# Performance work log

Hardware: AMD Instinct MI355X
Metric: run time of the kernel (lower is better)

The kernel has to match this reference:

```python
import jax, jax.numpy as jnp
import numpy as np

D_MODEL = 1024
D_STATE = 128
EXPAND = 2
HEADDIM = 64
D_CONV = 4
VAR_NUM = 3
D_INNER = EXPAND * D_MODEL            # 2048
NHEADS = D_INNER // HEADDIM           # 32
CONV_DIM = D_INNER + 2 * D_STATE      # 2304 (x, B, C share the conv)
D_IN_PROJ = 2 * D_INNER + 2 * D_STATE + NHEADS  # 4384


def setup_inputs() -> dict:
    key = jax.random.key(0)
    ks = jax.random.split(key, 10)
    s = 0.02
    B, L = 4, 2048
    return {
        "h_prev": jax.random.normal(ks[0], (B, L, D_MODEL), jnp.float32),
        "emb_next": jax.random.normal(ks[1], (B, L, D_MODEL), jnp.float32),
        "norm_w": jnp.ones((D_MODEL,), jnp.float32),
        "proj_W": jax.random.normal(ks[2], (D_MODEL, 2 * D_MODEL), jnp.float32) * s,
        "proj_b": jnp.zeros((D_MODEL,), jnp.float32),
        "in_proj_W": jax.random.normal(ks[3], (D_IN_PROJ, D_MODEL), jnp.float32) * s,
        "conv_w": jax.random.normal(ks[4], (CONV_DIM, D_CONV), jnp.float32) * s,
        "conv_b": jnp.zeros((CONV_DIM,), jnp.float32),
        "dt_bias": jax.random.uniform(ks[5], (NHEADS,), jnp.float32) * 0.1,
        "A_log": jnp.log(jnp.arange(1, NHEADS + 1, dtype=jnp.float32)),
        "D": jnp.ones((NHEADS,), jnp.float32),
        "gnorm_w": jnp.ones((D_INNER,), jnp.float32),
        "out_proj_W": jax.random.normal(ks[6], (D_MODEL, D_INNER), jnp.float32) * s,
        "dec_W": jax.random.normal(ks[7], (VAR_NUM, D_MODEL), jnp.float32) * s,
        "dec_b": jnp.zeros((VAR_NUM,), jnp.float32),
    }


def rmsnorm(x, w, eps=1e-6):
    xf = x.astype(jnp.float32)
    v = jnp.mean(jnp.square(xf), axis=-1, keepdims=True)
    return w * (xf * jax.lax.rsqrt(v + eps)).astype(x.dtype)


def gated_rmsnorm(y, z, w, eps=1e-5):
    y = y * jax.nn.silu(z)
    v = jnp.mean(jnp.square(y.astype(jnp.float32)), axis=-1, keepdims=True)
    return w * (y.astype(jnp.float32) * jax.lax.rsqrt(v + eps)).astype(y.dtype)


def mamba2(u, in_proj_W, conv_w, conv_b, dt_bias, A_log, D, gnorm_w, out_proj_W):
    B, L, _ = u.shape
    zxbcdt = u @ in_proj_W.T  # [B,L,D_IN_PROJ]
    z, xBC, dt = jnp.split(zxbcdt, [D_INNER, D_INNER + CONV_DIM], axis=-1)
    # causal depthwise conv over time
    lhs = jnp.moveaxis(xBC, -1, 1)               # [B,C,L]
    rhs = conv_w[:, None, :]                     # [C,1,K]
    conv = jax.lax.conv_general_dilated(lhs, rhs, (1,), [(D_CONV - 1, 0)],
                                        feature_group_count=CONV_DIM)
    xBC = jax.nn.silu(jnp.moveaxis(conv, 1, -1) + conv_b)
    x, Bm, Cm = jnp.split(xBC, [D_INNER, D_INNER + D_STATE], axis=-1)
    x = x.reshape(B, L, NHEADS, HEADDIM)         # [B,L,H,P]
    dt = jax.nn.softplus(dt + dt_bias)           # [B,L,H]
    A = -jnp.exp(A_log)                          # [H]
    dA = jnp.exp(dt * A)                         # [B,L,H]

    def step(state, inp):
        dA_t, dt_t, B_t, C_t, x_t = inp          # [B,H],[B,H],[B,N],[B,N],[B,H,P]
        state = state * dA_t[..., None, None] + (dt_t[..., None, None] * x_t[..., None]) * B_t[:, None, None, :]
        y_t = jnp.einsum('bhpn,bn->bhp', state, C_t)
        return state, y_t

    init = jnp.zeros((B, NHEADS, HEADDIM, D_STATE), u.dtype)
    xs = (jnp.moveaxis(dA, 1, 0), jnp.moveaxis(dt, 1, 0), jnp.moveaxis(Bm, 1, 0),
          jnp.moveaxis(Cm, 1, 0), jnp.moveaxis(x, 1, 0))
    _, y = jax.lax.scan(step, init, xs)          # y: [L,B,H,P]
    y = jnp.moveaxis(y, 0, 1) + D[None, None, :, None] * x
    y = y.reshape(B, L, D_INNER)
    y = gated_rmsnorm(y, z, gnorm_w)
    return y @ out_proj_W.T                      # [B,L,D_MODEL]


def reference(h_prev, emb_next, norm_w, proj_W, proj_b, in_proj_W, conv_w, conv_b,
              dt_bias, A_log, D, gnorm_w, out_proj_W, dec_W, dec_b):
    combined = jnp.concatenate([rmsnorm(h_prev, norm_w), rmsnorm(emb_next, norm_w)], axis=-1)
    h_prime = combined @ proj_W.T + proj_b       # [B,L,D_MODEL]
    h_k = mamba2(h_prime, in_proj_W, conv_w, conv_b, dt_bias, A_log, D, gnorm_w, out_proj_W)
    output = h_k @ dec_W.T + dec_b               # [B,L,VAR_NUM]
    return output, h_k
```

## Files before the change

### kernel.cpp

```cpp
#include <hip/hip_runtime.h>
#include <stdint.h>

#define T_TOK 8192
#define SEQL  2048
#define DM    1024
#define DI    2048
#define DSTATE 128
#define NH    32
#define HD    64
#define CONVD 2304
#define DINP  4384
#define LD_ZX 4480
#define QC    64
#define NCH   32

typedef __attribute__((ext_vector_type(8))) __bf16 bfrag;
typedef __attribute__((ext_vector_type(8))) short s16x8;
typedef __attribute__((ext_vector_type(4))) float f32x4;

__device__ __forceinline__ float bf2f(unsigned short u){
  return __uint_as_float(((unsigned)u) << 16);
}
__device__ __forceinline__ unsigned short f2bf(float f){
  unsigned u = __float_as_uint(f);
  unsigned r = (u + 0x7FFFu + ((u >> 16) & 1u)) >> 16;
  return (unsigned short)r;
}

__device__ __forceinline__ void gl_lds16(const unsigned short* g, unsigned short* l){
  __builtin_amdgcn_global_load_lds(
      (const __attribute__((address_space(1))) void*)g,
      (__attribute__((address_space(3))) void*)l,
      16, 0, 0);
}
__device__ __forceinline__ void gl_lds4(const float* g, float* l){
  __builtin_amdgcn_global_load_lds(
      (const __attribute__((address_space(1))) void*)g,
      (__attribute__((address_space(3))) void*)l,
      4, 0, 0);
}

__global__ __launch_bounds__(256) void cvt_w_kernel(const float* __restrict__ src,
                                                    unsigned short* __restrict__ dst,
                                                    int n4, int srcn4){
  int i = blockIdx.x * 256 + threadIdx.x;
  if (i >= n4) return;
  ushort4 o;
  if (i < srcn4){
    float4 v = ((const float4*)src)[i];
    o.x = f2bf(v.x); o.y = f2bf(v.y); o.z = f2bf(v.z); o.w = f2bf(v.w);
  } else {
    o.x = o.y = o.z = o.w = 0;
  }
  *(ushort4*)(dst + (size_t)i * 4) = o;
}

__global__ __launch_bounds__(256) void rmsnorm2_kernel(const float* __restrict__ a,
                                                       const float* __restrict__ b,
                                                       const float* __restrict__ w,
                                                       unsigned short* __restrict__ out){
  int t = blockIdx.x, tid = threadIdx.x;
  float4 va = *(const float4*)(a + (size_t)t * DM + tid * 4);
  float4 vb = *(const float4*)(b + (size_t)t * DM + tid * 4);
  float sa = va.x*va.x + va.y*va.y + va.z*va.z + va.w*va.w;
  float sb = vb.x*vb.x + vb.y*vb.y + vb.z*vb.z + vb.w*vb.w;
  #pragma unroll
  for (int o = 32; o; o >>= 1){ sa += __shfl_down(sa, o); sb += __shfl_down(sb, o); }
  __shared__ float reda[4], redb[4];
  int wv = tid >> 6, lane = tid & 63;
  if (!lane){ reda[wv] = sa; redb[wv] = sb; }
  __syncthreads();
  float ta = reda[0] + reda[1] + reda[2] + reda[3];
  float tb = redb[0] + redb[1] + redb[2] + redb[3];
  float ra = rsqrtf(ta * (1.f/1024.f) + 1e-6f);
  float rb = rsqrtf(tb * (1.f/1024.f) + 1e-6f);
  float4 vw = *(const float4*)(w + tid * 4);
  unsigned short* o0 = out + (size_t)t * DI + tid * 4;
  o0[0] = f2bf(va.x*ra*vw.x); o0[1] = f2bf(va.y*ra*vw.y);
  o0[2] = f2bf(va.z*ra*vw.z); o0[3] = f2bf(va.w*ra*vw.w);
  unsigned short* o1 = o0 + DM;
  o1[0] = f2bf(vb.x*rb*vw.x); o1[1] = f2bf(vb.y*rb*vw.y);
  o1[2] = f2bf(vb.z*rb*vw.z); o1[3] = f2bf(vb.w*rb*vw.w);
}

template<bool F32OUT>
__global__ __launch_bounds__(256) void gemm_bf16_kernel(const unsigned short* __restrict__ A,
                                                        const unsigned short* __restrict__ W,
                                                        void* __restrict__ Cv,
                                                        const float* __restrict__ bias,
                                                        int M, int N, int K, int ldc){
  __shared__ unsigned short As[128 * 64];
  __shared__ unsigned short Bs[128 * 64];
  const int nN = N >> 7;
  int bid = blockIdx.x;
  const int cpx = gridDim.x >> 3;
  bid = (bid & 7) * cpx + (bid >> 3);
  const int tm = bid / nN, tn = bid % nN;
  const int tid = threadIdx.x;
  const int wv = tid >> 6, lane = tid & 63;
  const int wm = wv >> 1, wn = wv & 1;
  const int rA = lane >> 3;
  const int cA = (lane & 7) << 3;
  const size_t arow0 = (size_t)(tm * 128) * K;
  const size_t brow0 = (size_t)(tn * 128) * K;

  f32x4 zero4 = {0.f, 0.f, 0.f, 0.f};
  f32x4 acc[4][4];
  #pragma unroll
  for (int i = 0; i < 4; ++i)
    #pragma unroll
    for (int j = 0; j < 4; ++j) acc[i][j] = zero4;

  const int nK = K >> 6;
  for (int kt = 0; kt < nK; ++kt){
    const int k0 = kt << 6;
    if (kt) __syncthreads();
    #pragma unroll
    for (int i = 0; i < 4; ++i){
      int base = (wv * 4 + i) * 8;
      gl_lds16(A + arow0 + (size_t)(base + rA) * K + k0 + cA, &As[base * 64]);
      gl_lds16(W + brow0 + (size_t)(base + rA) * K + k0 + cA, &Bs[base * 64]);
    }
    __syncthreads();
    #pragma unroll
    for (int kk = 0; kk < 2; ++kk){
      const int ko = kk * 32 + (lane >> 4) * 8;
      bfrag af[4], bfv[4];
      #pragma unroll
      for (int f = 0; f < 4; ++f){
        af[f]  = *reinterpret_cast<const bfrag*>(&As[(wm*64 + f*16 + (lane & 15)) * 64 + ko]);
        bfv[f] = *reinterpret_cast<const bfrag*>(&Bs[(wn*64 + f*16 + (lane & 15)) * 64 + ko]);
      }
      #pragma unroll
      for (int fm = 0; fm < 4; ++fm)
        #pragma unroll
        for (int fn = 0; fn < 4; ++fn)
          acc[fm][fn] = __builtin_amdgcn_mfma_f32_16x16x32_bf16(af[fm], bfv[fn], acc[fm][fn], 0, 0, 0);
    }
  }
  const int r0 = (lane >> 4) * 4, ci = lane & 15;
  #pragma unroll
  for (int fm = 0; fm < 4; ++fm){
    #pragma unroll
    for (int fn = 0; fn < 4; ++fn){
      int col = tn*128 + wn*64 + fn*16 + ci;
      float bv = bias ? bias[col] : 0.f;
      #pragma unroll
      for (int r = 0; r < 4; ++r){
        int row = tm*128 + wm*64 + fm*16 + r0 + r;
        float val = acc[fm][fn][r] + bv;
        if (F32OUT) ((float*)Cv)[(size_t)row * ldc + col] = val;
        else        ((unsigned short*)Cv)[(size_t)row * ldc + col] = f2bf(val);
      }
    }
  }
}

__global__ __launch_bounds__(256) void conv_kernel(const unsigned short* __restrict__ zx,
                                                   const float* __restrict__ cw,
                                                   const float* __restrict__ cb,
                                                   unsigned short* __restrict__ xbc){
  int c = blockIdx.x * 256 + threadIdx.x;
  int tg = blockIdx.y * 8;
  int l0 = tg & (SEQL - 1);
  const unsigned short* base = zx + (size_t)tg * LD_ZX + DI + c;
  float v[11];
  #pragma unroll
  for (int i = 0; i < 11; ++i){
    int ll = l0 - 3 + i;
    v[i] = (ll >= 0) ? bf2f(base[(ptrdiff_t)(i - 3) * LD_ZX]) : 0.f;
  }
  float w0 = cw[c*4+0], w1 = cw[c*4+1], w2 = cw[c*4+2], w3 = cw[c*4+3];
  float cbv = cb[c];
  unsigned short* ob = xbc + (size_t)tg * CONVD + c;
  #pragma unroll
  for (int s = 0; s < 8; ++s){
    float acc = cbv + w0*v[s] + w1*v[s+1] + w2*v[s+2] + w3*v[s+3];
    float sv = acc / (1.f + expf(-acc));
    ob[(size_t)s * CONVD] = f2bf(sv);
  }
}

__global__ __launch_bounds__(256) void cum_kernel(const unsigned short* __restrict__ zx,
                                                  const float* __restrict__ dtbias,
                                                  const float* __restrict__ alog,
                                                  float* __restrict__ cumT,
                                                  float* __restrict__ dtT,
                                                  float* __restrict__ decayG){
  int gw = blockIdx.x * 4 + (threadIdx.x >> 6);
  int l = threadIdx.x & 63;
  int c = gw & 31, h = (gw >> 5) & 31, b = gw >> 10;
  size_t t = (size_t)b * SEQL + c * QC + l;
  float xr = bf2f(zx[t * LD_ZX + 4352 + h]) + dtbias[h];
  float dt = (xr > 20.f) ? xr : log1pf(expf(xr));
  float A = -expf(alog[h]);
  float x = dt * A;
  #pragma unroll
  for (int d = 1; d < 64; d <<= 1){
    float y = __shfl_up(x, d);
    if (l >= d) x += y;
  }
  size_t o = ((size_t)(b * NH + h)) * SEQL + c * QC + l;
  cumT[o] = x;
  dtT[o] = dt;
  float tot = __shfl(x, 63);
  if (l == 0) decayG[(b * NH + h) * NCH + c] = expf(tot);
}

__global__ __launch_bounds__(256) void chunk_dS_kernel(const unsigned short* __restrict__ xbc,
                                                       const float* __restrict__ cumT,
                                                       const float* __restrict__ dtT,
                                                       unsigned short* __restrict__ dS){
  __shared__ unsigned short Xw[64 * 64];
  __shared__ unsigned short Bt[128 * 64];
  __shared__ float cumS[64], dtS[64];
  const int blk = blockIdx.x;
  const int c = blk & 31, h = (blk >> 5) & 31, b = blk >> 10;
  const int tid = threadIdx.x;
  const int wv = tid >> 6, l = tid & 63;
  const size_t tokB = (size_t)b * SEQL + c * QC;
  const int bh = b * NH + h;

  if (wv == 0) gl_lds4(cumT + (size_t)bh * SEQL + c * QC + l, cumS);
  if (wv == 1) gl_lds4(dtT  + (size_t)bh * SEQL + c * QC + l, dtS);

  const int j = tid >> 2, g4 = tid & 3;
  const unsigned short* xsrc = xbc + (tokB + j) * CONVD + h * HD + g4 * 16;
  s16x8 x0 = *(const s16x8*)xsrc, x1 = *(const s16x8*)(xsrc + 8);
  const unsigned short* bsrc = xbc + (tokB + j) * CONVD + DI + g4 * 32;
  s16x8 b0 = *(const s16x8*)bsrc,        b1 = *(const s16x8*)(bsrc + 8);
  s16x8 b2 = *(const s16x8*)(bsrc + 16), b3 = *(const s16x8*)(bsrc + 24);
  __syncthreads();

  float wj = expf(cumS[63] - cumS[j]) * dtS[j];
  const int jh = (j >> 3), jl = (j & 7);
  #pragma unroll
  for (int e = 0; e < 8; ++e){
    int p = g4 * 16 + e;
    Xw[p * 64 + ((jh ^ (p & 7)) << 3) + jl] = f2bf(bf2f((unsigned short)x0[e]) * wj);
    int p2 = p + 8;
    Xw[p2 * 64 + ((jh ^ (p2 & 7)) << 3) + jl] = f2bf(bf2f((unsigned short)x1[e]) * wj);
  }
  #pragma unroll
  for (int e = 0; e < 8; ++e){
    int n0 = g4 * 32 + e;
    Bt[(n0     ) * 64 + ((jh ^ ((n0     ) & 7)) << 3) + jl] = (unsigned short)b0[e];
    Bt[(n0 +  8) * 64 + ((jh ^ ((n0 +  8) & 7)) << 3) + jl] = (unsigned short)b1[e];
    Bt[(n0 + 16) * 64 + ((jh ^ ((n0 + 16) & 7)) << 3) + jl] = (unsigned short)b2[e];
    Bt[(n0 + 24) * 64 + ((jh ^ ((n0 + 24) & 7)) << 3) + jl] = (unsigned short)b3[e];
  }
  __syncthreads();

  f32x4 z4 = {0.f,0.f,0.f,0.f};
  f32x4 acc[4][2];
  #pragma unroll
  for (int pt = 0; pt < 4; ++pt){ acc[pt][0] = z4; acc[pt][1] = z4; }
  #pragma unroll
  for (int ks = 0; ks < 2; ++ks){
    const int au = ((ks * 4 + (l >> 4)) ^ (l & 7));
    bfrag a[4], bb[2];
    #pragma unroll
    for (int pt = 0; pt < 4; ++pt)
      a[pt] = *(const bfrag*)&Xw[(pt * 16 + (l & 15)) * 64 + au * 8];
    #pragma unroll
    for (int nt = 0; nt < 2; ++nt)
      bb[nt] = *(const bfrag*)&Bt[((wv * 2 + nt) * 16 + (l & 15)) * 64 + au * 8];
    #pragma unroll
    for (int pt = 0; pt < 4; ++pt)
      #pragma unroll
      for (int nt = 0; nt < 2; ++nt)
        acc[pt][nt] = __builtin_amdgcn_mfma_f32_16x16x32_bf16(a[pt], bb[nt], acc[pt][nt], 0, 0, 0);
  }
  unsigned short* out = dS + ((size_t)(bh * NCH + c) * 64) * 128;
  #pragma unroll
  for (int pt = 0; pt < 4; ++pt)
    #pragma unroll
    for (int nt = 0; nt < 2; ++nt)
      #pragma unroll
      for (int r = 0; r < 4; ++r){
        int p = pt * 16 + (l >> 4) * 4 + r;
        int n = (wv * 2 + nt) * 16 + (l & 15);
        out[(size_t)p * 128 + n] = f2bf(acc[pt][nt][r]);
      }
}

__global__ __launch_bounds__(256) void chunk_state_kernel(const float* __restrict__ decayG,
                                                          unsigned short* __restrict__ dS){
  int i = blockIdx.x * 256 + threadIdx.x;
  int n = i & 127, p = (i >> 7) & 63, bh = i >> 13;
  float s = 0.f;
  #pragma unroll 4
  for (int c = 0; c < NCH; ++c){
    size_t idx = ((size_t)(bh * NCH + c) * 64 + p) * 128 + n;
    unsigned short d = dS[idx];
    dS[idx] = f2bf(s);
    s = decayG[bh * NCH + c] * s + bf2f(d);
  }
}

__global__ __launch_bounds__(256) void chunk_Y_kernel(const unsigned short* __restrict__ xbc,
                                                      const unsigned short* __restrict__ Sb,
                                                      const float* __restrict__ cumT,
                                                      const float* __restrict__ dtT,
                                                      const float* __restrict__ Dvec,
                                                      unsigned short* __restrict__ ybuf){
  __shared__ unsigned short Cs[64 * 128];
  __shared__ unsigned short Bs[64 * 128];
  __shared__ unsigned short Xt[64 * 64];
  __shared__ unsigned short Ms[64 * 64];
  __shared__ float cumS[64], dtS[64];
  const int blk = blockIdx.x;
  const int c = blk & 31, h = (blk >> 5) & 31, b = blk >> 10;
  const int tid = threadIdx.x;
  const int wv = tid >> 6, l = tid & 63;
  const size_t tokB = (size_t)b * SEQL + c * QC;
  const int bh = b * NH + h;

  #pragma unroll
  for (int kk = 0; kk < 4; ++kk){
    int k = wv * 4 + kk;
    int row = k * 4 + (l >> 4);
    int us = (l & 15) ^ (row & 7);
    gl_lds16(xbc + (tokB + row) * CONVD + 2176 + us * 8, &Cs[k * 512]);
    gl_lds16(xbc + (tokB + row) * CONVD + 2048 + us * 8, &Bs[k * 512]);
  }
  if (wv == 0) gl_lds4(cumT + (size_t)bh * SEQL + c * QC + l, cumS);
  if (wv == 1) gl_lds4(dtT  + (size_t)bh * SEQL + c * QC + l, dtS);

  {
    const int j = tid >> 2, g4 = tid & 3;
    const unsigned short* xsrc = xbc + (tokB + j) * CONVD + h * HD + g4 * 16;
    s16x8 x0 = *(const s16x8*)xsrc, x1 = *(const s16x8*)(xsrc + 8);
    const int jh = j >> 3, jl = j & 7;
    #pragma unroll
    for (int e = 0; e < 8; ++e){
      int p = g4 * 16 + e;
      Xt[p * 64 + ((jh ^ (p & 7)) << 3) + jl] = (unsigned short)x0[e];
      int p2 = p + 8;
      Xt[p2 * 64 + ((jh ^ (p2 & 7)) << 3) + jl] = (unsigned short)x1[e];
    }
  }
  __syncthreads();

  bfrag sbf[4][4];
  {
    const unsigned short* sbase = Sb + (size_t)(bh * NCH + c) * 64 * 128;
    #pragma unroll
    for (int pt = 0; pt < 4; ++pt)
      #pragma unroll
      for (int ks = 0; ks < 4; ++ks){
        int p = pt * 16 + (l & 15);
        sbf[pt][ks] = *(const bfrag*)(sbase + (size_t)p * 128 + ks * 32 + (l >> 4) * 8);
      }
  }

  f32x4 z4 = {0.f,0.f,0.f,0.f};
  f32x4 macc[4] = {z4, z4, z4, z4};
  #pragma unroll
  for (int ks = 0; ks < 4; ++ks){
    const int au = (ks * 4 + (l >> 4)) ^ (l & 7);
    bfrag ca = *(const bfrag*)&Cs[(wv * 16 + (l & 15)) * 128 + au * 8];
    #pragma unroll
    for (int jt = 0; jt < 4; ++jt){
      bfrag bb = *(const bfrag*)&Bs[(jt * 16 + (l & 15)) * 128 + au * 8];
      macc[jt] = __builtin_amdgcn_mfma_f32_16x16x32_bf16(ca, bb, macc[jt], 0, 0, 0);
    }
  }
  float cj[4], dj[4];
  #pragma unroll
  for (int jt = 0; jt < 4; ++jt){
    int jv = jt * 16 + (l & 15);
    cj[jt] = cumS[jv]; dj[jt] = dtS[jv];
  }
  float ctv[4];
  #pragma unroll
  for (int r = 0; r < 4; ++r) ctv[r] = cumS[wv * 16 + (l >> 4) * 4 + r];
  #pragma unroll
  for (int jt = 0; jt < 4; ++jt){
    int jv = jt * 16 + (l & 15);
    #pragma unroll
    for (int r = 0; r < 4; ++r){
      int tb = wv * 16 + (l >> 4) * 4 + r;
      float g = (jv <= tb) ? expf(ctv[r] - cj[jt]) * dj[jt] : 0.f;
      Ms[tb * 64 + (((jv >> 3) ^ (tb & 7)) << 3) + (jv & 7)] = f2bf(macc[jt][r] * g);
    }
  }
  f32x4 yacc[4] = {z4, z4, z4, z4};
  #pragma unroll
  for (int kj = 0; kj < 2; ++kj){
    const int au = (kj * 4 + (l >> 4)) ^ (l & 7);
    bfrag ma = *(const bfrag*)&Ms[(wv * 16 + (l & 15)) * 64 + au * 8];
    #pragma unroll
    for (int pt = 0; pt < 4; ++pt){
      bfrag wx = *(const bfrag*)&Xt[(pt * 16 + (l & 15)) * 64 + au * 8];
      yacc[pt] = __builtin_amdgcn_mfma_f32_16x16x32_bf16(ma, wx, yacc[pt], 0, 0, 0);
    }
  }
  f32x4 iacc[4] = {z4, z4, z4, z4};
  #pragma unroll
  for (int ks = 0; ks < 4; ++ks){
    const int au = (ks * 4 + (l >> 4)) ^ (l & 7);
    bfrag ca = *(const bfrag*)&Cs[(wv * 16 + (l & 15)) * 128 + au * 8];
    #pragma unroll
    for (int pt = 0; pt < 4; ++pt)
      iacc[pt] = __builtin_amdgcn_mfma_f32_16x16x32_bf16(ca, sbf[pt][ks], iacc[pt], 0, 0, 0);
  }
  const float Dh = Dvec[h];
  float er[4];
  #pragma unroll
  for (int r = 0; r < 4; ++r) er[r] = expf(ctv[r]);
  #pragma unroll
  for (int pt = 0; pt < 4; ++pt)
    #pragma unroll
    for (int r = 0; r < 4; ++r){
      int p = pt * 16 + (l & 15);
      int tb = wv * 16 + (l >> 4) * 4 + r;
      float xv = bf2f(Xt[p * 64 + (((tb >> 3) ^ (p & 7)) << 3) + (tb & 7)]);
      float yv = yacc[pt][r] + er[r] * iacc[pt][r] + Dh * xv;
      ybuf[(tokB + tb) * DI + h * HD + p] = f2bf(yv);
    }
}

__global__ __launch_bounds__(256) void gated_kernel(const unsigned short* __restrict__ y,
                                                    const unsigned short* __restrict__ zx,
                                                    const float* __restrict__ gw,
                                                    unsigned short* __restrict__ out){
  int t = blockIdx.x, tid = threadIdx.x;
  s16x8 yv = *(const s16x8*)(y  + (size_t)t * DI    + tid * 8);
  s16x8 zv = *(const s16x8*)(zx + (size_t)t * LD_ZX + tid * 8);
  float g[8]; float ss = 0.f;
  #pragma unroll
  for (int j = 0; j < 8; ++j){
    float yf = bf2f((unsigned short)yv[j]);
    float zf = bf2f((unsigned short)zv[j]);
    float gi = yf * (zf / (1.f + expf(-zf)));
    g[j] = gi; ss += gi * gi;
  }
  #pragma unroll
  for (int o = 32; o; o >>= 1) ss += __shfl_down(ss, o);
  __shared__ float red[4];
  int wv = tid >> 6, lane = tid & 63;
  if (!lane) red[wv] = ss;
  __syncthreads();
  float tot = red[0] + red[1] + red[2] + red[3];
  float sc = rsqrtf(tot * (1.f/2048.f) + 1e-5f);
  unsigned short* o0 = out + (size_t)t * DI + tid * 8;
  #pragma unroll
  for (int j = 0; j < 8; ++j) o0[j] = f2bf(g[j] * sc * gw[tid * 8 + j]);
}

__global__ __launch_bounds__(256) void dec_kernel(const float* __restrict__ hk,
                                                  const float* __restrict__ dw,
                                                  const float* __restrict__ db,
                                                  float* __restrict__ out){
  int t = (blockIdx.x * 256 + threadIdx.x) >> 6;
  int lane = threadIdx.x & 63;
  const float* hr = hk + (size_t)t * DM + lane * 16;
  float h[16];
  #pragma unroll
  for (int j = 0; j < 16; ++j) h[j] = hr[j];
  float a0 = 0.f, a1 = 0.f, a2 = 0.f;
  const float* w0 = dw + lane * 16;
  const float* w1 = dw + DM + lane * 16;
  const float* w2 = dw + 2 * DM + lane * 16;
  #pragma unroll
  for (int j = 0; j < 16; ++j){
    a0 = fmaf(h[j], w0[j], a0);
    a1 = fmaf(h[j], w1[j], a1);
    a2 = fmaf(h[j], w2[j], a2);
  }
  #pragma unroll
  for (int o = 32; o; o >>= 1){
    a0 += __shfl_down(a0, o);
    a1 += __shfl_down(a1, o);
    a2 += __shfl_down(a2, o);
  }
  if (!lane){
    out[t * 3 + 0] = a0 + db[0];
    out[t * 3 + 1] = a1 + db[1];
    out[t * 3 + 2] = a2 + db[2];
  }
}

extern "C" void kernel_launch(void* const* d_in, const int* in_sizes, int n_in,
                              void* d_out, int out_size, void* d_ws, size_t ws_size,
                              hipStream_t stream){
  const float* h_prev    = (const float*)d_in[0];
  const float* emb_next  = (const float*)d_in[1];
  const float* norm_w    = (const float*)d_in[2];
  const float* proj_W    = (const float*)d_in[3];
  const float* proj_b    = (const float*)d_in[4];
  const float* in_proj_W = (const float*)d_in[5];
  const float* conv_w    = (const float*)d_in[6];
  const float* conv_b    = (const float*)d_in[7];
  const float* dt_bias   = (const float*)d_in[8];
  const float* A_log     = (const float*)d_in[9];
  const float* Dvec      = (const float*)d_in[10];
  const float* gnorm_w   = (const float*)d_in[11];
  const float* out_proj_W= (const float*)d_in[12];
  const float* dec_W     = (const float*)d_in[13];
  const float* dec_b     = (const float*)d_in[14];

  char* ws = (char*)d_ws;
  size_t off = 0;
  auto take = [&](size_t bytes){ char* p = ws + off; off += (bytes + 255) & ~(size_t)255; return p; };
  unsigned short* wproj = (unsigned short*)take((size_t)DM * DI * 2);
  unsigned short* winp  = (unsigned short*)take((size_t)LD_ZX * DM * 2);
  unsigned short* wout  = (unsigned short*)take((size_t)DM * DI * 2);
  unsigned short* zx    = (unsigned short*)take((size_t)T_TOK * LD_ZX * 2);
  float*          cumT  = (float*)take((size_t)4 * NH * SEQL * 4);
  float*          dtT   = (float*)take((size_t)4 * NH * SEQL * 4);
  float*          decayG= (float*)take((size_t)4 * NH * NCH * 4);
  char* regionA = take((size_t)T_TOK * CONVD * 2);
  unsigned short* combined = (unsigned short*)regionA;
  unsigned short* xbc      = (unsigned short*)regionA;
  char* regionY = take((size_t)T_TOK * DI * 2);
  unsigned short* hprime = (unsigned short*)regionY;
  unsigned short* ybuf   = (unsigned short*)regionY;
  unsigned short* dS = (unsigned short*)take((size_t)128 * NCH * 64 * 128 * 2);

  float* outp = (float*)d_out;
  float* hk   = outp + (size_t)T_TOK * 3;

  cvt_w_kernel<<<2048, 256, 0, stream>>>(proj_W, wproj, DM*DI/4, DM*DI/4);
  cvt_w_kernel<<<4480, 256, 0, stream>>>(in_proj_W, winp, LD_ZX*DM/4, DINP*DM/4);
  cvt_w_kernel<<<2048, 256, 0, stream>>>(out_proj_W, wout, DM*DI/4, DM*DI/4);

  rmsnorm2_kernel<<<T_TOK, 256, 0, stream>>>(h_prev, emb_next, norm_w, combined);

  gemm_bf16_kernel<false><<<(T_TOK/128)*(DM/128), 256, 0, stream>>>(combined, wproj, hprime, proj_b,
                                                                    T_TOK, DM, DI, DM);
  gemm_bf16_kernel<false><<<(T_TOK/128)*(LD_ZX/128), 256, 0, stream>>>(hprime, winp, zx, nullptr,
                                                                       T_TOK, LD_ZX, DM, LD_ZX);
  conv_kernel<<<dim3(CONVD/256, T_TOK/8), 256, 0, stream>>>(zx, conv_w, conv_b, xbc);
  cum_kernel<<<1024, 256, 0, stream>>>(zx, dt_bias, A_log, cumT, dtT, decayG);
  chunk_dS_kernel<<<4096, 256, 0, stream>>>(xbc, cumT, dtT, dS);
  chunk_state_kernel<<<4096, 256, 0, stream>>>(decayG, dS);
  chunk_Y_kernel<<<4096, 256, 0, stream>>>(xbc, dS, cumT, dtT, Dvec, ybuf);
  gated_kernel<<<T_TOK, 256, 0, stream>>>(ybuf, zx, gnorm_w, ybuf);
  gemm_bf16_kernel<true><<<(T_TOK/128)*(DM/128), 256, 0, stream>>>(ybuf, wout, hk, nullptr,
                                                                   T_TOK, DM, DI, DM);
  dec_kernel<<<T_TOK/4, 256, 0, stream>>>(hk, dec_W, dec_b, outp);
}
```

Measured before the change: 402.0 us.

## Add 256x128 triple-buffered GEMM for in_proj and vectorize chunk state scan

Adds a new 512-thread GEMM kernel with 256x128 tiles, a three-stage global-to-LDS pipeline, XOR-swizzled shared memory, grid swizzling and MFMA priority hints, and uses it for the in_proj GEMM. The aim is better data reuse and latency hiding on the largest projection. Separately, the inter-chunk state scan now processes 8 state elements per thread with 16-byte vector loads and stores, so it launches fewer blocks and moves memory more efficiently. The larger tile uses more LDS and registers per block, which lowers occupancy.

```diff
diff --git a/kernel.cpp b/kernel.cpp
--- a/kernel.cpp
+++ b/kernel.cpp
@@ -156,6 +156,132 @@
   }
 }
 
+__global__ __launch_bounds__(512, 1) void gemm4f_kernel(const unsigned short* __restrict__ A,
+                                                        const unsigned short* __restrict__ W,
+                                                        unsigned short* __restrict__ C,
+                                                        int M, int N, int K, int ldc){
+  __shared__ unsigned short As[3][256 * 64];
+  __shared__ unsigned short Bs[3][128 * 64];
+  const int nN = N >> 7;
+  int bid = blockIdx.x;
+  const int cpx = gridDim.x >> 3;
+  bid = (bid & 7) * cpx + (bid >> 3);
+  const int tm = bid / nN, tn = bid % nN;
+  const int tid = threadIdx.x;
+  const int wv = tid >> 6, l = tid & 63;
+  const int wm = wv >> 1, wn = wv & 1;
+  const size_t arow0 = (size_t)(tm * 256) * K;
+  const size_t brow0 = (size_t)(tn * 128) * K;
+  const int nK = K >> 6;
+
+  int asrc[4], bsrc[2];
+  #pragma unroll
+  for (int i = 0; i < 4; ++i){
+    int d = (i * 8 + wv) * 64 + l;
+    int row = d >> 3, ul = (d & 7) ^ (row & 7);
+    asrc[i] = row * K + ul * 8;
+  }
+  #pragma unroll
+  for (int i = 0; i < 2; ++i){
+    int d = (i * 8 + wv) * 64 + l;
+    int row = d >> 3, ul = (d & 7) ^ (row & 7);
+    bsrc[i] = row * K + ul * 8;
+  }
+  int aoff[4][2], boff[4][2];
+  #pragma unroll
+  for (int m = 0; m < 4; ++m)
+    #pragma unroll
+    for (int ks = 0; ks < 2; ++ks){
+      int row = wm * 64 + m * 16 + (l & 15);
+      int u = (ks * 4 + (l >> 4)) ^ (row & 7);
+      aoff[m][ks] = row * 64 + u * 8;
+    }
+  #pragma unroll
+  for (int n = 0; n < 4; ++n)
+    #pragma unroll
+    for (int ks = 0; ks < 2; ++ks){
+      int row = wn * 64 + n * 16 + (l & 15);
+      int u = (ks * 4 + (l >> 4)) ^ (row & 7);
+      boff[n][ks] = row * 64 + u * 8;
+    }
+
+  f32x4 acc[4][4];
+  #pragma unroll
+  for (int m = 0; m < 4; ++m)
+    #pragma unroll
+    for (int n = 0; n < 4; ++n) acc[m][n] = (f32x4){0.f,0.f,0.f,0.f};
+
+  auto stage = [&](int vt){
+    int kt = vt > nK - 1 ? nK - 1 : vt;
+    const int s = vt % 3;
+    const int k0 = kt << 6;
+    #pragma unroll
+    for (int i = 0; i < 4; ++i)
+      gl_lds16(A + arow0 + k0 + asrc[i], &As[s][(i * 8 + wv) * 512]);
+    #pragma unroll
+    for (int i = 0; i < 2; ++i)
+      gl_lds16(W + brow0 + k0 + bsrc[i], &Bs[s][(i * 8 + wv) * 512]);
+  };
+
+  stage(0); stage(1);
+  asm volatile("s_waitcnt vmcnt(6)" ::: "memory");
+  __builtin_amdgcn_s_barrier();
+
+  for (int t = 0; t < nK; ++t){
+    stage(t + 2);
+    asm volatile("s_waitcnt vmcnt(12)" ::: "memory");
+    __builtin_amdgcn_s_barrier();
+    __builtin_amdgcn_sched_barrier(0);
+    const unsigned short* Ab = &As[t % 3][0];
+    const unsigned short* Bb = &Bs[t % 3][0];
+    bfrag bf0[4], bf1[4];
+    #pragma unroll
+    for (int n = 0; n < 4; ++n){
+      bf0[n] = *(const bfrag*)&Bb[boff[n][0]];
+      bf1[n] = *(const bfrag*)&Bb[boff[n][1]];
+    }
+    #pragma unroll
+    for (int h = 0; h < 2; ++h){
+      bfrag a00 = *(const bfrag*)&Ab[aoff[2*h][0]];
+      bfrag a01 = *(const bfrag*)&Ab[aoff[2*h][1]];
+      bfrag a10 = *(const bfrag*)&Ab[aoff[2*h+1][0]];
+      bfrag a11 = *(const bfrag*)&Ab[aoff[2*h+1][1]];
+      __builtin_amdgcn_s_barrier();
+      asm volatile("s_waitcnt lgkmcnt(0)" ::: "memory");
+      __builtin_amdgcn_sched_barrier(0);
+      __builtin_amdgcn_s_setprio(1);
+      #pragma unroll
+      for (int n = 0; n < 4; ++n)
+        acc[2*h][n] = __builtin_amdgcn_mfma_f32_16x16x32_bf16(a00, bf0[n], acc[2*h][n], 0, 0, 0);
+      #pragma unroll
+      for (int n = 0; n < 4; ++n)
+        acc[2*h][n] = __builtin_amdgcn_mfma_f32_16x16x32_bf16(a01, bf1[n], acc[2*h][n], 0, 0, 0);
+      #pragma unroll
+      for (int n = 0; n < 4; ++n)
+        acc[2*h+1][n] = __builtin_amdgcn_mfma_f32_16x16x32_bf16(a10, bf0[n], acc[2*h+1][n], 0, 0, 0);
+      #pragma unroll
+      for (int n = 0; n < 4; ++n)
+        acc[2*h+1][n] = __builtin_amdgcn_mfma_f32_16x16x32_bf16(a11, bf1[n], acc[2*h+1][n], 0, 0, 0);
+      __builtin_amdgcn_s_setprio(0);
+      __builtin_amdgcn_s_barrier();
+    }
+  }
+
+  const int r0 = (l >> 4) * 4, ci = l & 15;
+  #pragma unroll
+  for (int m = 0; m < 4; ++m){
+    #pragma unroll
+    for (int n = 0; n < 4; ++n){
+      const int col = tn*128 + wn*64 + n*16 + ci;
+      #pragma unroll
+      for (int r = 0; r < 4; ++r){
+        const int row = tm*256 + wm*64 + m*16 + r0 + r;
+        C[(size_t)row * ldc + col] = f2bf(acc[m][n][r]);
+      }
+    }
+  }
+}
+
 __global__ __launch_bounds__(256) void conv_kernel(const unsigned short* __restrict__ zx,
                                                    const float* __restrict__ cw,
                                                    const float* __restrict__ cb,
@@ -287,14 +413,21 @@
 __global__ __launch_bounds__(256) void chunk_state_kernel(const float* __restrict__ decayG,
                                                           unsigned short* __restrict__ dS){
   int i = blockIdx.x * 256 + threadIdx.x;
-  int n = i & 127, p = (i >> 7) & 63, bh = i >> 13;
-  float s = 0.f;
-  #pragma unroll 4
+  int n8 = i & 15, p = (i >> 4) & 63, bh = i >> 10;
+  float s[8];
+  #pragma unroll
+  for (int j = 0; j < 8; ++j) s[j] = 0.f;
+  const float* dg = decayG + bh * NCH;
   for (int c = 0; c < NCH; ++c){
-    size_t idx = ((size_t)(bh * NCH + c) * 64 + p) * 128 + n;
-    unsigned short d = dS[idx];
-    dS[idx] = f2bf(s);
-    s = decayG[bh * NCH + c] * s + bf2f(d);
+    size_t idx = ((size_t)(bh * NCH + c) * 64 + p) * 128 + n8 * 8;
+    s16x8 d = *(const s16x8*)(dS + idx);
+    s16x8 o;
+    #pragma unroll
+    for (int j = 0; j < 8; ++j) o[j] = (short)f2bf(s[j]);
+    *(s16x8*)(dS + idx) = o;
+    float g = dg[c];
+    #pragma unroll
+    for (int j = 0; j < 8; ++j) s[j] = fmaf(g, s[j], bf2f((unsigned short)d[j]));
   }
 }
 
@@ -530,12 +663,12 @@
 
   gemm_bf16_kernel<false><<<(T_TOK/128)*(DM/128), 256, 0, stream>>>(combined, wproj, hprime, proj_b,
                                                                     T_TOK, DM, DI, DM);
-  gemm_bf16_kernel<false><<<(T_TOK/128)*(LD_ZX/128), 256, 0, stream>>>(hprime, winp, zx, nullptr,
-                                                                       T_TOK, LD_ZX, DM, LD_ZX);
+  gemm4f_kernel<<<(T_TOK/256)*(LD_ZX/128), 512, 0, stream>>>(hprime, winp, zx,
+                                                             T_TOK, LD_ZX, DM, LD_ZX);
   conv_kernel<<<dim3(CONVD/256, T_TOK/8), 256, 0, stream>>>(zx, conv_w, conv_b, xbc);
   cum_kernel<<<1024, 256, 0, stream>>>(zx, dt_bias, A_log, cumT, dtT, decayG);
   chunk_dS_kernel<<<4096, 256, 0, stream>>>(xbc, cumT, dtT, dS);
-  chunk_state_kernel<<<4096, 256, 0, stream>>>(decayG, dS);
+  chunk_state_kernel<<<512, 256, 0, stream>>>(decayG, dS);
   chunk_Y_kernel<<<4096, 256, 0, stream>>>(xbc, dS, cumT, dtT, Dvec, ybuf);
   gated_kernel<<<T_TOK, 256, 0, stream>>>(ybuf, zx, gnorm_w, ybuf);
   gemm_bf16_kernel<true><<<(T_TOK/128)*(DM/128), 256, 0, stream>>>(ybuf, wout, hk, nullptr,
```

Result: slower. 427.9 us (+6.5%).
